# Performance work log

Hardware: AMD Instinct MI355X
Metric: run time of the kernel (lower is better)

## Reference

```python
import jax, jax.numpy as jnp
import numpy as np

FEATURE_DIM = 1024
HEAD_NUM = 16
HIDDEN_DIM = FEATURE_DIM // HEAD_NUM


def setup_inputs() -> dict:
    key = jax.random.key(0)
    ks = jax.random.split(key, 12)
    B, S, D = 4, 2048, FEATURE_DIM
    s = 1.0 / np.sqrt(D)
    inp = {
        "query": jax.random.normal(ks[0], (B, S, D), jnp.float32),
        "key": jax.random.normal(ks[1], (B, S, D), jnp.float32),
        "value": jax.random.normal(ks[2], (B, S, D), jnp.float32),
        "mask": jax.random.randint(ks[3], (B, 1, 1, S), 0, 2, jnp.int32),
        "Wq": jax.random.normal(ks[4], (D, D), jnp.float32) * s,
        "bq": jnp.zeros((D,), jnp.float32),
        "Wk": jax.random.normal(ks[5], (D, D), jnp.float32) * s,
        "bk": jnp.zeros((D,), jnp.float32),
        "Wv": jax.random.normal(ks[6], (D, D), jnp.float32) * s,
        "bv": jnp.zeros((D,), jnp.float32),
        "Wo": jax.random.normal(ks[7], (D, D), jnp.float32) * s,
        "bo": jnp.zeros((D,), jnp.float32),
    }
    return inp


def reference(query, key, value, mask, Wq, bq, Wk, bk, Wv, bv, Wo, bo):
    B, Sq, D = query.shape
    H, Hd = HEAD_NUM, HIDDEN_DIM
    scale = jnp.sqrt(jnp.asarray(Hd, query.dtype))

    def split_heads(x):
        b, s, _ = x.shape
        return x.reshape(b, s, H, Hd).transpose(0, 2, 1, 3)  # [B,H,S,Hd]

    Q = split_heads(query @ Wq.T + bq)
    K = split_heads(key @ Wk.T + bk)
    V = split_heads(value @ Wv.T + bv)

    scores = jnp.einsum("bhqd,bhkd->bhqk", Q, K) / scale
    scores = jnp.where(mask == 0, jnp.asarray(-1e10, scores.dtype), scores)
    attn = jax.nn.softmax(scores, axis=-1)  # dropout p=0 -> identity
    h = jnp.einsum("bhqk,bhkd->bhqd", attn, V)
    h = h.transpose(0, 2, 1, 3).reshape(B, Sq, D)
    return h @ Wo.T + bo
```

## Files before the change

kernel.cpp:

```cpp
#include <hip/hip_runtime.h>
#include <hip/hip_bf16.h>
#include <cstdint>
#include <cstddef>

#define D_MODEL 1024
#define SEQ     2048
#define BATCH   4
#define NHEAD   16
#define HD      64
#define MROWS   (BATCH * SEQ)

typedef __attribute__((ext_vector_type(8))) short  short8;
typedef __attribute__((ext_vector_type(4))) float  floatx4;
typedef __attribute__((ext_vector_type(4))) unsigned short ushort4v;
typedef unsigned short u16;

__device__ __forceinline__ u16 f2bf(float x) {
    __hip_bfloat16 h = __float2bfloat16(x);
    return *(u16*)&h;
}

__device__ __forceinline__ void async_copy16(const u16* g, u16* l) {
    __builtin_amdgcn_global_load_lds(
        (const __attribute__((address_space(1))) void*)g,
        (__attribute__((address_space(3))) void*)l, 16, 0, 0);
}

__device__ __forceinline__ void cvt8(const float* s, u16* d, size_t i) {
    const float4 a = *(const float4*)(s + i);
    const float4 b = *(const float4*)(s + i + 4);
    short8 o;
    o[0] = (short)f2bf(a.x); o[1] = (short)f2bf(a.y);
    o[2] = (short)f2bf(a.z); o[3] = (short)f2bf(a.w);
    o[4] = (short)f2bf(b.x); o[5] = (short)f2bf(b.y);
    o[6] = (short)f2bf(b.z); o[7] = (short)f2bf(b.w);
    *(short8*)(d + i) = o;
}

__global__ __launch_bounds__(256) void cvt4(
    const float* __restrict__ s0, const float* __restrict__ s1,
    const float* __restrict__ s2, const float* __restrict__ s3,
    u16* __restrict__ d0, u16* __restrict__ d1,
    u16* __restrict__ d2, u16* __restrict__ d3)
{
    const float* s = blockIdx.y == 0 ? s0 : (blockIdx.y == 1 ? s1 :
                     (blockIdx.y == 2 ? s2 : s3));
    u16*         d = blockIdx.y == 0 ? d0 : (blockIdx.y == 1 ? d1 :
                     (blockIdx.y == 2 ? d2 : d3));
    cvt8(s, d, ((size_t)blockIdx.x * 256 + threadIdx.x) * 8);
}

__global__ __launch_bounds__(256) void gemm_qkv(
    const float* __restrict__ Aq, const float* __restrict__ Ak,
    const float* __restrict__ Av,
    const u16* __restrict__ Wqp, const u16* __restrict__ Wkp,
    const u16* __restrict__ Wvp,
    const float* __restrict__ bqp, const float* __restrict__ bkp,
    const float* __restrict__ bvp,
    u16* __restrict__ oq, u16* __restrict__ ok, u16* __restrict__ ov)
{
    constexpr int K = D_MODEL;
    __shared__ __align__(16) u16 smem[16384];
    u16 (*As)[64] = (u16(*)[64])smem;
    u16 (*Ws)[64] = (u16(*)[64])(smem + 8192);

    const int z = blockIdx.z;
    const float* A    = z == 0 ? Aq  : (z == 1 ? Ak  : Av);
    const u16*   W    = z == 0 ? Wqp : (z == 1 ? Wkp : Wvp);
    const float* bias = z == 0 ? bqp : (z == 1 ? bkp : bvp);
    u16*         out  = z == 0 ? oq  : (z == 1 ? ok  : ov);

    const int bm = blockIdx.x * 128;
    const int bn = blockIdx.y * 128;
    const int t  = threadIdx.x;
    const int w  = t >> 6;
    const int l  = t & 63;
    const int li = l & 15;
    const int quad = l >> 4;
    const int wm = (w & 1) * 64;
    const int wn = (w >> 1) * 64;
    const int srow = w * 32 + (l >> 3);
    const int lc8  = (l & 7) * 8;

    const float* Ab = A + (size_t)bm * K;
    const u16*   Wb = W + (size_t)bn * K;

    float4 pa[4][2];
    short8 pw[4];
    #pragma unroll
    for (int j = 0; j < 4; j++) {
        const float* ap = Ab + (size_t)(srow + j * 8) * K + lc8;
        pa[j][0] = *(const float4*)ap;
        pa[j][1] = *(const float4*)(ap + 4);
        pw[j] = *(const short8*)(Wb + (size_t)(srow + j * 8) * K + lc8);
    }

    floatx4 acc[4][4];
    #pragma unroll
    for (int mi = 0; mi < 4; mi++)
        #pragma unroll
        for (int ni = 0; ni < 4; ni++) acc[mi][ni] = (floatx4){0.f,0.f,0.f,0.f};

    for (int kt = 0; kt < K; kt += 64) {
        __syncthreads();
        #pragma unroll
        for (int j = 0; j < 4; j++) {
            short8 av;
            av[0] = (short)f2bf(pa[j][0].x); av[1] = (short)f2bf(pa[j][0].y);
            av[2] = (short)f2bf(pa[j][0].z); av[3] = (short)f2bf(pa[j][0].w);
            av[4] = (short)f2bf(pa[j][1].x); av[5] = (short)f2bf(pa[j][1].y);
            av[6] = (short)f2bf(pa[j][1].z); av[7] = (short)f2bf(pa[j][1].w);
            *(short8*)&As[srow + j * 8][lc8] = av;
            *(short8*)&Ws[srow + j * 8][lc8] = pw[j];
        }
        __syncthreads();
        if (kt + 64 < K) {
            #pragma unroll
            for (int j = 0; j < 4; j++) {
                const float* ap = Ab + (size_t)(srow + j * 8) * K + kt + 64 + lc8;
                pa[j][0] = *(const float4*)ap;
                pa[j][1] = *(const float4*)(ap + 4);
                pw[j] = *(const short8*)(Wb + (size_t)(srow + j * 8) * K + kt + 64 + lc8);
            }
        }
        #pragma unroll
        for (int ks = 0; ks < 2; ks++) {
            short8 af[4], bf[4];
            #pragma unroll
            for (int i = 0; i < 4; i++) {
                af[i] = *(const short8*)&As[wm + i * 16 + li][ks * 32 + quad * 8];
                bf[i] = *(const short8*)&Ws[wn + i * 16 + li][ks * 32 + quad * 8];
            }
            #pragma unroll
            for (int mi = 0; mi < 4; mi++)
                #pragma unroll
                for (int ni = 0; ni < 4; ni++)
                    acc[mi][ni] = __builtin_amdgcn_mfma_f32_16x16x32_bf16(
                        af[mi], bf[ni], acc[mi][ni], 0, 0, 0);
        }
    }

    if (z < 2) {
        #pragma unroll
        for (int mi = 0; mi < 4; mi++)
            #pragma unroll
            for (int ni = 0; ni < 4; ni++) {
                const int c  = bn + wn + ni * 16 + li;
                const int h  = c >> 6;
                const int hd = c & 63;
                const float bz = bias[c];
                #pragma unroll
                for (int reg = 0; reg < 4; reg++) {
                    const int r = bm + wm + mi * 16 + quad * 4 + reg;
                    const int b = r >> 11;
                    const int s = r & (SEQ - 1);
                    out[(((size_t)(b * NHEAD + h) * SEQ) + s) * HD + hd] = f2bf(acc[mi][ni][reg] + bz);
                }
            }
    } else {
        u16 (*Ct)[128] = (u16(*)[128])smem;
        __syncthreads();
        #pragma unroll
        for (int mi = 0; mi < 4; mi++)
            #pragma unroll
            for (int ni = 0; ni < 4; ni++) {
                const int cl = wn + ni * 16 + li;
                const float bz = bias[bn + cl];
                #pragma unroll
                for (int reg = 0; reg < 4; reg++) {
                    const int rl = wm + mi * 16 + quad * 4 + reg;
                    Ct[cl][rl] = f2bf(acc[mi][ni][reg] + bz);
                }
            }
        __syncthreads();
        const int cl   = t >> 1;
        const int half = t & 1;
        const int cg = bn + cl;
        const int h  = cg >> 6;
        const int hd = cg & 63;
        const int b  = bm >> 11;
        const int s0 = (bm & (SEQ - 1)) + half * 64;
        u16* dst = out + (((size_t)(b * NHEAD + h) * HD) + hd) * SEQ + s0;
        const short8* sp = (const short8*)&Ct[cl][half * 64];
        #pragma unroll
        for (int i = 0; i < 8; i++) ((short8*)dst)[i] = sp[i];
    }
}

__global__ __launch_bounds__(256) void gemm_out(
    const u16* __restrict__ A,
    const u16* __restrict__ W,
    const float* __restrict__ bias,
    float* __restrict__ out)
{
    constexpr int K = D_MODEL;
    __shared__ __align__(16) u16 smem[16384];
    u16 (*As)[64] = (u16(*)[64])smem;
    u16 (*Ws)[64] = (u16(*)[64])(smem + 8192);

    const int bm = blockIdx.x * 128;
    const int bn = blockIdx.y * 128;
    const int t  = threadIdx.x;
    const int w  = t >> 6;
    const int l  = t & 63;
    const int li = l & 15;
    const int quad = l >> 4;
    const int wm = (w & 1) * 64;
    const int wn = (w >> 1) * 64;
    const int lrow = l >> 3;
    const int lcol = (l & 7) * 8;

    const u16* Ag = A + (size_t)bm * K;
    const u16* Wg = W + (size_t)bn * K;

    floatx4 acc[4][4];
    #pragma unroll
    for (int mi = 0; mi < 4; mi++)
        #pragma unroll
        for (int ni = 0; ni < 4; ni++) acc[mi][ni] = (floatx4){0.f,0.f,0.f,0.f};

    for (int kt = 0; kt < K; kt += 64) {
        __syncthreads();
        #pragma unroll
        for (int j = 0; j < 4; j++) {
            const int r = w * 32 + j * 8;
            async_copy16(Ag + (size_t)(r + lrow) * K + kt + lcol, &As[r][0]);
            async_copy16(Wg + (size_t)(r + lrow) * K + kt + lcol, &Ws[r][0]);
        }
        __syncthreads();

        #pragma unroll
        for (int ks = 0; ks < 2; ks++) {
            short8 af[4], bf[4];
            #pragma unroll
            for (int i = 0; i < 4; i++) {
                af[i] = *(const short8*)&As[wm + i * 16 + li][ks * 32 + quad * 8];
                bf[i] = *(const short8*)&Ws[wn + i * 16 + li][ks * 32 + quad * 8];
            }
            #pragma unroll
            for (int mi = 0; mi < 4; mi++)
                #pragma unroll
                for (int ni = 0; ni < 4; ni++)
                    acc[mi][ni] = __builtin_amdgcn_mfma_f32_16x16x32_bf16(
                        af[mi], bf[ni], acc[mi][ni], 0, 0, 0);
        }
    }

    #pragma unroll
    for (int mi = 0; mi < 4; mi++)
        #pragma unroll
        for (int ni = 0; ni < 4; ni++) {
            const int c = bn + wn + ni * 16 + li;
            const float bz = bias[c];
            #pragma unroll
            for (int reg = 0; reg < 4; reg++) {
                const int r = bm + wm + mi * 16 + quad * 4 + reg;
                out[(size_t)r * D_MODEL + c] = acc[mi][ni][reg] + bz;
            }
        }
}

#define LOG2E   1.44269504088896340736f
#define CSCALE  (0.125f * LOG2E)

__global__ __launch_bounds__(256) void attn_mfma(
    const u16* __restrict__ Q,
    const u16* __restrict__ K,
    const u16* __restrict__ Vt,
    const int* __restrict__ mask,
    u16* __restrict__ H)
{
    __shared__ __align__(16) u16 Ks[2][64 * 64];
    __shared__ __align__(16) u16 Vs[2][64 * 64];
    __shared__ __align__(16) u16 Ps[4][32][72];
    __shared__ float mc[2][64];

    const int bh  = blockIdx.y;
    const int b   = bh >> 4;
    const int h   = bh & 15;
    const int q0  = blockIdx.x * 128;
    const int t   = threadIdx.x;
    const int w   = t >> 6;
    const int l   = t & 63;
    const int li  = l & 15;
    const int quad  = l >> 4;
    const int lrow8 = l >> 3;
    const int gch   = (l & 7) ^ lrow8;
    const int swz   = li & 7;

    short8 qf[2][2];
    #pragma unroll
    for (int qb = 0; qb < 2; qb++) {
        const u16* Qrow = Q + ((size_t)bh * SEQ + q0 + w * 32 + qb * 16 + li) * HD;
        qf[qb][0] = *(const short8*)(Qrow + quad * 8);
        qf[qb][1] = *(const short8*)(Qrow + 32 + quad * 8);
    }

    const u16* Kbh = K  + (size_t)bh * SEQ * HD;
    const u16* Vbh = Vt + (size_t)bh * HD * SEQ;
    const int* mg  = mask + (size_t)b * SEQ;

    floatx4 oacc[4][2];
    #pragma unroll
    for (int hm = 0; hm < 4; hm++)
        #pragma unroll
        for (int qb = 0; qb < 2; qb++) oacc[hm][qb] = (floatx4){0.f,0.f,0.f,0.f};
    float rs[2] = {0.f, 0.f};

    #pragma unroll
    for (int j = 0; j < 2; j++) {
        const int rb = w * 16 + j * 8;
        async_copy16(Kbh + (size_t)(rb + lrow8) * HD + gch * 8, &Ks[0][rb * 64]);
        async_copy16(Vbh + (size_t)(rb + lrow8) * SEQ + gch * 8, &Vs[0][rb * 64]);
    }
    if (t < 64) mc[0][t] = (mg[t] != 0) ? -16.0f : -1.0e9f;

    int cur = 0;
    for (int kt = 0; kt < SEQ; kt += 64) {
        __syncthreads();
        if (kt + 64 < SEQ) {
            const int nb_ = cur ^ 1;
            #pragma unroll
            for (int j = 0; j < 2; j++) {
                const int rb = w * 16 + j * 8;
                async_copy16(Kbh + (size_t)(kt + 64 + rb + lrow8) * HD + gch * 8,
                             &Ks[nb_][rb * 64]);
                async_copy16(Vbh + (size_t)(rb + lrow8) * SEQ + kt + 64 + gch * 8,
                             &Vs[nb_][rb * 64]);
            }
            if (t < 64) mc[nb_][t] = (mg[kt + 64 + t] != 0) ? -16.0f : -1.0e9f;
        }

        floatx4 sacc[4][2];
        #pragma unroll
        for (int kb = 0; kb < 4; kb++)
            #pragma unroll
            for (int qb = 0; qb < 2; qb++) sacc[kb][qb] = (floatx4){0.f,0.f,0.f,0.f};
        #pragma unroll
        for (int ks = 0; ks < 2; ks++) {
            short8 kf[4];
            #pragma unroll
            for (int kb = 0; kb < 4; kb++)
                kf[kb] = *(const short8*)&Ks[cur][(kb * 16 + li) * 64 + ((ks * 4 + quad) ^ swz) * 8];
            #pragma unroll
            for (int kb = 0; kb < 4; kb++)
                #pragma unroll
                for (int qb = 0; qb < 2; qb++)
                    sacc[kb][qb] = __builtin_amdgcn_mfma_f32_16x16x32_bf16(
                        kf[kb], qf[qb][ks], sacc[kb][qb], 0, 0, 0);
        }

        #pragma unroll
        for (int kb = 0; kb < 4; kb++) {
            const float4 m4 = *(const float4*)&mc[cur][kb * 16 + quad * 4];
            #pragma unroll
            for (int qb = 0; qb < 2; qb++) {
                const float p0 = __builtin_amdgcn_exp2f(fmaf(sacc[kb][qb][0], CSCALE, m4.x));
                const float p1 = __builtin_amdgcn_exp2f(fmaf(sacc[kb][qb][1], CSCALE, m4.y));
                const float p2 = __builtin_amdgcn_exp2f(fmaf(sacc[kb][qb][2], CSCALE, m4.z));
                const float p3 = __builtin_amdgcn_exp2f(fmaf(sacc[kb][qb][3], CSCALE, m4.w));
                rs[qb] += (p0 + p1) + (p2 + p3);
                ushort4v pk;
                pk[0] = f2bf(p0); pk[1] = f2bf(p1);
                pk[2] = f2bf(p2); pk[3] = f2bf(p3);
                *(ushort4v*)&Ps[w][qb * 16 + li][kb * 16 + quad * 4] = pk;
            }
        }

        #pragma unroll
        for (int ks = 0; ks < 2; ks++) {
            short8 pf[2];
            #pragma unroll
            for (int qb = 0; qb < 2; qb++)
                pf[qb] = *(const short8*)&Ps[w][qb * 16 + li][ks * 32 + quad * 8];
            #pragma unroll
            for (int hm = 0; hm < 4; hm++) {
                const short8 vf = *(const short8*)&Vs[cur][(hm * 16 + li) * 64 + ((ks * 4 + quad) ^ swz) * 8];
                #pragma unroll
                for (int qb = 0; qb < 2; qb++)
                    oacc[hm][qb] = __builtin_amdgcn_mfma_f32_16x16x32_bf16(
                        vf, pf[qb], oacc[hm][qb], 0, 0, 0);
            }
        }
        cur ^= 1;
    }

    float linv[2];
    #pragma unroll
    for (int qb = 0; qb < 2; qb++) {
        float v = rs[qb];
        v += __shfl_xor(v, 16, 64);
        v += __shfl_xor(v, 32, 64);
        linv[qb] = 1.0f / v;
    }
    #pragma unroll
    for (int qb = 0; qb < 2; qb++) {
        const size_t row = (size_t)b * SEQ + q0 + w * 32 + qb * 16 + li;
        #pragma unroll
        for (int hm = 0; hm < 4; hm++) {
            ushort4v o;
            #pragma unroll
            for (int reg = 0; reg < 4; reg++)
                o[reg] = f2bf(oacc[hm][qb][reg] * linv[qb]);
            *(ushort4v*)&H[row * D_MODEL + h * 64 + hm * 16 + quad * 4] = o;
        }
    }
}

extern "C" void kernel_launch(void* const* d_in, const int* in_sizes, int n_in,
                              void* d_out, int out_size, void* d_ws, size_t ws_size,
                              hipStream_t stream)
{
    const float* query = (const float*)d_in[0];
    const float* key_  = (const float*)d_in[1];
    const float* value = (const float*)d_in[2];
    const int*   mask  = (const int*)  d_in[3];
    const float* Wq = (const float*)d_in[4];
    const float* bq = (const float*)d_in[5];
    const float* Wk = (const float*)d_in[6];
    const float* bk = (const float*)d_in[7];
    const float* Wv = (const float*)d_in[8];
    const float* bv = (const float*)d_in[9];
    const float* Wo = (const float*)d_in[10];
    const float* bo = (const float*)d_in[11];
    float* out = (float*)d_out;

    const size_t per = (size_t)BATCH * NHEAD * SEQ * HD;
    const size_t wsz = (size_t)D_MODEL * D_MODEL;
    u16* Qb  = (u16*)d_ws;
    u16* Kb  = Qb  + per;
    u16* Vtb = Kb  + per;
    u16* Hb  = Vtb + per;
    u16* Wqb = Hb  + per;
    u16* Wkb = Wqb + wsz;
    u16* Wvb = Wkb + wsz;
    u16* Wob = Wvb + wsz;

    cvt4<<<dim3(wsz / 2048, 4), 256, 0, stream>>>(Wq, Wk, Wv, Wo,
                                                  Wqb, Wkb, Wvb, Wob);

    gemm_qkv<<<dim3(MROWS / 128, D_MODEL / 128, 3), 256, 0, stream>>>(
        query, key_, value, Wqb, Wkb, Wvb, bq, bk, bv, Qb, Kb, Vtb);

    attn_mfma<<<dim3(SEQ / 128, BATCH * NHEAD), 256, 0, stream>>>(
        Qb, Kb, Vtb, mask, Hb);

    gemm_out<<<dim3(MROWS / 128, D_MODEL / 128), 256, 0, stream>>>(
        Hb, Wob, bo, out);
}
```

Baseline: 381.2 us.

## Single-buffer K/V with staggered loads and raise MFMA wave priority

Replaces the double-buffered K/V/mask tiles in the attention kernel with single buffers. V for the current tile now loads during the QK^T and softmax phase, and the next K tile plus mask load during the PV phase, separated by an extra barrier per iteration. This roughly halves the K/V shared-memory footprint, which may allow more resident blocks per CU. It also wraps the MFMA loops in s_setprio so matrix work gets scheduling priority. The cost is a second __syncthreads per key tile and less prefetch distance, since each load has only about half an iteration to complete.

```diff
diff --git a/kernel.cpp b/kernel.cpp
--- a/kernel.cpp
+++ b/kernel.cpp
@@ -270,10 +270,10 @@
     const int* __restrict__ mask,
     u16* __restrict__ H)
 {
-    __shared__ __align__(16) u16 Ks[2][64 * 64];
-    __shared__ __align__(16) u16 Vs[2][64 * 64];
+    __shared__ __align__(16) u16 Ks[64 * 64];
+    __shared__ __align__(16) u16 Vs[64 * 64];
     __shared__ __align__(16) u16 Ps[4][32][72];
-    __shared__ float mc[2][64];
+    __shared__ __align__(16) float mc[64];
 
     const int bh  = blockIdx.y;
     const int b   = bh >> 4;
@@ -310,25 +310,18 @@
     #pragma unroll
     for (int j = 0; j < 2; j++) {
         const int rb = w * 16 + j * 8;
-        async_copy16(Kbh + (size_t)(rb + lrow8) * HD + gch * 8, &Ks[0][rb * 64]);
-        async_copy16(Vbh + (size_t)(rb + lrow8) * SEQ + gch * 8, &Vs[0][rb * 64]);
-    }
-    if (t < 64) mc[0][t] = (mg[t] != 0) ? -16.0f : -1.0e9f;
-
-    int cur = 0;
+        async_copy16(Kbh + (size_t)(rb + lrow8) * HD + gch * 8, &Ks[rb * 64]);
+    }
+    if (t < 64) mc[t] = (mg[t] != 0) ? -16.0f : -1.0e9f;
+
     for (int kt = 0; kt < SEQ; kt += 64) {
         __syncthreads();
-        if (kt + 64 < SEQ) {
-            const int nb_ = cur ^ 1;
-            #pragma unroll
-            for (int j = 0; j < 2; j++) {
-                const int rb = w * 16 + j * 8;
-                async_copy16(Kbh + (size_t)(kt + 64 + rb + lrow8) * HD + gch * 8,
-                             &Ks[nb_][rb * 64]);
-                async_copy16(Vbh + (size_t)(rb + lrow8) * SEQ + kt + 64 + gch * 8,
-                             &Vs[nb_][rb * 64]);
-            }
-            if (t < 64) mc[nb_][t] = (mg[kt + 64 + t] != 0) ? -16.0f : -1.0e9f;
+
+        #pragma unroll
+        for (int j = 0; j < 2; j++) {
+            const int rb = w * 16 + j * 8;
+            async_copy16(Vbh + (size_t)(rb + lrow8) * SEQ + kt + gch * 8,
+                         &Vs[rb * 64]);
         }
 
         floatx4 sacc[4][2];
@@ -341,18 +334,20 @@
             short8 kf[4];
             #pragma unroll
             for (int kb = 0; kb < 4; kb++)
-                kf[kb] = *(const short8*)&Ks[cur][(kb * 16 + li) * 64 + ((ks * 4 + quad) ^ swz) * 8];
+                kf[kb] = *(const short8*)&Ks[(kb * 16 + li) * 64 + ((ks * 4 + quad) ^ swz) * 8];
+            __builtin_amdgcn_s_setprio(1);
             #pragma unroll
             for (int kb = 0; kb < 4; kb++)
                 #pragma unroll
                 for (int qb = 0; qb < 2; qb++)
                     sacc[kb][qb] = __builtin_amdgcn_mfma_f32_16x16x32_bf16(
                         kf[kb], qf[qb][ks], sacc[kb][qb], 0, 0, 0);
+            __builtin_amdgcn_s_setprio(0);
         }
 
         #pragma unroll
         for (int kb = 0; kb < 4; kb++) {
-            const float4 m4 = *(const float4*)&mc[cur][kb * 16 + quad * 4];
+            const float4 m4 = *(const float4*)&mc[kb * 16 + quad * 4];
             #pragma unroll
             for (int qb = 0; qb < 2; qb++) {
                 const float p0 = __builtin_amdgcn_exp2f(fmaf(sacc[kb][qb][0], CSCALE, m4.x));
@@ -367,22 +362,35 @@
             }
         }
 
+        __syncthreads();
+
+        if (kt + 64 < SEQ) {
+            #pragma unroll
+            for (int j = 0; j < 2; j++) {
+                const int rb = w * 16 + j * 8;
+                async_copy16(Kbh + (size_t)(kt + 64 + rb + lrow8) * HD + gch * 8,
+                             &Ks[rb * 64]);
+            }
+            if (t < 64) mc[t] = (mg[kt + 64 + t] != 0) ? -16.0f : -1.0e9f;
+        }
+
         #pragma unroll
         for (int ks = 0; ks < 2; ks++) {
             short8 pf[2];
             #pragma unroll
             for (int qb = 0; qb < 2; qb++)
                 pf[qb] = *(const short8*)&Ps[w][qb * 16 + li][ks * 32 + quad * 8];
+            __builtin_amdgcn_s_setprio(1);
             #pragma unroll
             for (int hm = 0; hm < 4; hm++) {
-                const short8 vf = *(const short8*)&Vs[cur][(hm * 16 + li) * 64 + ((ks * 4 + quad) ^ swz) * 8];
+                const short8 vf = *(const short8*)&Vs[(hm * 16 + li) * 64 + ((ks * 4 + quad) ^ swz) * 8];
                 #pragma unroll
                 for (int qb = 0; qb < 2; qb++)
                     oacc[hm][qb] = __builtin_amdgcn_mfma_f32_16x16x32_bf16(
                         vf, pf[qb], oacc[hm][qb], 0, 0, 0);
             }
-        }
-        cur ^= 1;
+            __builtin_amdgcn_s_setprio(0);
+        }
     }
 
     float linv[2];
```

After: 371.1 us. -2.7%, faster.
